# Kernel tuning notes

Measured on AMD Instinct MI355X. Metric: run time of the kernel, lower is better.

The kernel has to match this reference:

```python
import jax, jax.numpy as jnp
import numpy as np

B, L, H, K = 16, 512, 1024, 8192

def setup_inputs() -> dict:
    key = jax.random.key(0)
    k1, k2 = jax.random.split(key)
    inputs = jax.random.normal(k1, (B, L, H), dtype=jnp.float32)
    masks = jnp.ones((B, L), dtype=bool)
    # xavier_uniform for Linear(hidden_size, labels_num): weight [K, H]
    limit = float(np.sqrt(6.0 / (H + K)))
    W = jax.random.uniform(k2, (K, H), dtype=jnp.float32, minval=-limit, maxval=limit)
    return {"inputs": inputs, "masks": masks, "W": W}

def reference(inputs, masks, W):
    # scores: [B, K, L] = (inputs @ W.T).transpose(1,2)
    scores = jnp.einsum('blh,kh->bkl', inputs, W)
    scores = jnp.where(masks[:, None, :], scores, -jnp.inf)
    attn = jax.nn.softmax(scores, axis=-1)          # softmax over L
    return jnp.einsum('bkl,blh->bkh', attn, inputs)  # [B, K, H]
```

## Files before the change

kernel.cpp:

```cpp
#include <hip/hip_runtime.h>
#include <stdint.h>

#define BN 16
#define LN 512
#define HN 1024
#define KN 8192
#define TK 64
#define NTHREADS 512

typedef float  f32x4  __attribute__((ext_vector_type(4)));
typedef __bf16 bf16x8 __attribute__((ext_vector_type(8)));
typedef __bf16 bf16x4 __attribute__((ext_vector_type(4)));

__device__ __forceinline__ void cp16(const void* g, void* l) {
  __builtin_amdgcn_global_load_lds(
      (const __attribute__((address_space(1))) unsigned int*)g,
      (__attribute__((address_space(3))) unsigned int*)l, 16, 0, 0);
}

__global__ void cvt_w(const float* __restrict__ W, __bf16* __restrict__ Wb) {
  const size_t i = (size_t)blockIdx.x * blockDim.x + threadIdx.x;
  const float4 v = ((const float4*)W)[i];
  bf16x4 o; o[0] = (__bf16)v.x; o[1] = (__bf16)v.y; o[2] = (__bf16)v.z; o[3] = (__bf16)v.w;
  ((bf16x4*)Wb)[i] = o;
}

__global__ void trans_x(const float* __restrict__ X, __bf16* __restrict__ Xb,
                        __bf16* __restrict__ Xt) {
  __shared__ __bf16 T[64][72];
  const int b  = blockIdx.y;
  const int l0 = (blockIdx.x & 7) * 64;
  const int h0 = (blockIdx.x >> 3) * 64;
  const int t  = threadIdx.x;
  #pragma unroll
  for (int it = 0; it < 4; ++it) {
    const int idx = it * 256 + t;
    const int lr = idx >> 4, hc = (idx & 15) << 2;
    const float4 v = *(const float4*)(X + ((size_t)b * LN + l0 + lr) * HN + h0 + hc);
    bf16x4 o; o[0] = (__bf16)v.x; o[1] = (__bf16)v.y; o[2] = (__bf16)v.z; o[3] = (__bf16)v.w;
    *(bf16x4*)(Xb + ((size_t)b * LN + l0 + lr) * HN + h0 + hc) = o;
    *(bf16x4*)&T[lr][hc] = o;
  }
  __syncthreads();
  #pragma unroll
  for (int it = 0; it < 4; ++it) {
    const int idx = it * 256 + t;
    const int hr = idx >> 4, lg = (idx & 15) << 2;
    bf16x4 o;
    o[0] = T[lg + 0][hr]; o[1] = T[lg + 1][hr];
    o[2] = T[lg + 2][hr]; o[3] = T[lg + 3][hr];
    *(bf16x4*)(Xt + ((size_t)b * HN + h0 + hr) * LN + l0 + lg) = o;
  }
}

#define P2_AT_LDA 520

struct __align__(16) P1Mem {
  __bf16 xs[2][512 * 64];
  __bf16 wt[2][64 * 64];
};
struct __align__(16) P2Mem {
  __bf16 attn[TK][P2_AT_LDA];
  __bf16 xt[2][512 * 32];
};
struct __align__(16) SMem {
  union {
    P1Mem p1;
    P2Mem p2;
    float osm[TK * 516];
  } u;
  float redM[8][TK];
  float redS[8][TK];
  float Mf[TK];
  float Sinv[TK];
};

__global__ __launch_bounds__(NTHREADS, 1)
void mlattn_fused2(const __bf16* __restrict__ Wb, const __bf16* __restrict__ Xb,
                   const __bf16* __restrict__ Xt, const int* __restrict__ Mk,
                   float* __restrict__ out) {
  __shared__ SMem sm;
  const int t    = threadIdx.x;
  const int wv   = t >> 6;
  const int lane = t & 63;
  const int q    = lane >> 4;
  const int c    = lane & 15;
  const int b    = blockIdx.y;
  const int k0   = blockIdx.x * TK;
  const __bf16* Xbb = Xb + (size_t)b * LN * HN;
  const __bf16* Xtb = Xt + (size_t)b * HN * LN;
  const f32x4 fzero = {0.f, 0.f, 0.f, 0.f};

  const int tr8 = t >> 3, tc8 = t & 7;
  const int colOff1 = ((tc8 ^ (tr8 & 7)) << 3);
  const __bf16* xsrc = Xbb + (size_t)tr8 * HN + colOff1;
  const __bf16* wsrc = Wb + (size_t)(k0 + tr8) * HN + colOff1;
  const int tr4 = t >> 2, tc4 = t & 3;
  const int colOff2 = ((tc4 ^ ((t >> 3) & 3)) << 3);
  const __bf16* tsrc = Xtb + (size_t)tr4 * LN + colOff2;

  f32x4 acc[4][4];
  #pragma unroll
  for (int mt = 0; mt < 4; ++mt)
    #pragma unroll
    for (int nt = 0; nt < 4; ++nt) acc[mt][nt] = fzero;

  const int lw0 = wv * 64;

  {
    cp16(wsrc, &sm.u.p1.wt[0][t * 8]);
    #pragma unroll
    for (int i = 0; i < 8; ++i)
      cp16(xsrc + (size_t)i * 64 * HN, &sm.u.p1.xs[0][(i * 512 + t) * 8]);
  }
  __syncthreads();

  int cur = 0;
  for (int tt = 0; tt < 16; ++tt) {
    if (tt + 1 < 16) {
      const int h0 = (tt + 1) * 64;
      cp16(wsrc + h0, &sm.u.p1.wt[cur ^ 1][t * 8]);
      #pragma unroll
      for (int i = 0; i < 8; ++i)
        cp16(xsrc + (size_t)i * 64 * HN + h0, &sm.u.p1.xs[cur ^ 1][(i * 512 + t) * 8]);
    }
    #pragma unroll
    for (int ks = 0; ks < 2; ++ks) {
      bf16x8 aF[4], bF[4];
      #pragma unroll
      for (int mt = 0; mt < 4; ++mt) {
        const int r = mt * 16 + c;
        aF[mt] = *(const bf16x8*)&sm.u.p1.wt[cur][r * 64 + (((ks * 4 + q) ^ (c & 7)) << 3)];
      }
      #pragma unroll
      for (int nt = 0; nt < 4; ++nt) {
        const int r = lw0 + nt * 16 + c;
        bF[nt] = *(const bf16x8*)&sm.u.p1.xs[cur][r * 64 + (((ks * 4 + q) ^ (c & 7)) << 3)];
      }
      #pragma unroll
      for (int mt = 0; mt < 4; ++mt)
        #pragma unroll
        for (int nt = 0; nt < 4; ++nt)
          acc[mt][nt] = __builtin_amdgcn_mfma_f32_16x16x32_bf16(aF[mt], bF[nt], acc[mt][nt], 0, 0, 0);
    }
    __syncthreads();
    cur ^= 1;
  }

  {
    #pragma unroll
    for (int i = 0; i < 4; ++i)
      cp16(tsrc + (size_t)i * 128 * LN, &sm.u.p2.xt[0][(i * 512 + t) * 8]);
  }

  #pragma unroll
  for (int nt = 0; nt < 4; ++nt) {
    const int m = Mk[b * LN + lw0 + nt * 16 + c];
    if (!m) {
      #pragma unroll
      for (int mt = 0; mt < 4; ++mt)
        #pragma unroll
        for (int r = 0; r < 4; ++r) acc[mt][nt][r] = -1e30f;
    }
  }
  float pm[4][4];
  #pragma unroll
  for (int mt = 0; mt < 4; ++mt)
    #pragma unroll
    for (int r = 0; r < 4; ++r)
      pm[mt][r] = fmaxf(fmaxf(acc[mt][0][r], acc[mt][1][r]), fmaxf(acc[mt][2][r], acc[mt][3][r]));
  #pragma unroll
  for (int off = 1; off < 16; off <<= 1)
    #pragma unroll
    for (int mt = 0; mt < 4; ++mt)
      #pragma unroll
      for (int r = 0; r < 4; ++r)
        pm[mt][r] = fmaxf(pm[mt][r], __shfl_xor(pm[mt][r], off, 64));
  if (c == 0) {
    #pragma unroll
    for (int mt = 0; mt < 4; ++mt)
      #pragma unroll
      for (int r = 0; r < 4; ++r) sm.redM[wv][mt * 16 + q * 4 + r] = pm[mt][r];
  }
  __syncthreads();
  if (t < TK) {
    float m = sm.redM[0][t];
    #pragma unroll
    for (int w = 1; w < 8; ++w) m = fmaxf(m, sm.redM[w][t]);
    sm.Mf[t] = m;
  }
  __syncthreads();

  float ps[4][4];
  #pragma unroll
  for (int mt = 0; mt < 4; ++mt)
    #pragma unroll
    for (int r = 0; r < 4; ++r) {
      const float M = sm.Mf[mt * 16 + q * 4 + r];
      float s = 0.f;
      #pragma unroll
      for (int nt = 0; nt < 4; ++nt) {
        const float e = __expf(acc[mt][nt][r] - M);
        acc[mt][nt][r] = e;
        s += e;
      }
      ps[mt][r] = s;
    }
  #pragma unroll
  for (int off = 1; off < 16; off <<= 1)
    #pragma unroll
    for (int mt = 0; mt < 4; ++mt)
      #pragma unroll
      for (int r = 0; r < 4; ++r) ps[mt][r] += __shfl_xor(ps[mt][r], off, 64);
  if (c == 0) {
    #pragma unroll
    for (int mt = 0; mt < 4; ++mt)
      #pragma unroll
      for (int r = 0; r < 4; ++r) sm.redS[wv][mt * 16 + q * 4 + r] = ps[mt][r];
  }
  __syncthreads();
  if (t < TK) {
    float s = 0.f;
    #pragma unroll
    for (int w = 0; w < 8; ++w) s += sm.redS[w][t];
    sm.Sinv[t] = 1.f / s;
  }
  __syncthreads();

  #pragma unroll
  for (int mt = 0; mt < 4; ++mt)
    #pragma unroll
    for (int r = 0; r < 4; ++r) {
      const int row = mt * 16 + q * 4 + r;
      const float inv = sm.Sinv[row];
      #pragma unroll
      for (int nt = 0; nt < 4; ++nt)
        sm.u.p2.attn[row][lw0 + nt * 16 + c] = (__bf16)(acc[mt][nt][r] * inv);
    }
  __syncthreads();

  const int wM = wv >> 2;
  const int wN = wv & 3;
  const int swq8 = ((q ^ ((c >> 1) & 3)) << 3);
  f32x4 acc2[2][16];
  #pragma unroll
  for (int i = 0; i < 2; ++i)
    #pragma unroll
    for (int j = 0; j < 16; ++j) acc2[i][j] = fzero;

  cur = 0;
  for (int s = 0; s < 32; ++s) {
    if (s + 1 < 32) {
      const int sn = s + 1;
      const __bf16* src = tsrc + (size_t)((sn & 1) * 512) * LN + ((sn >> 1) << 5);
      #pragma unroll
      for (int i = 0; i < 4; ++i)
        cp16(src + (size_t)i * 128 * LN, &sm.u.p2.xt[cur ^ 1][(i * 512 + t) * 8]);
    }
    const int l0c = (s >> 1) << 5;
    const int hh  = s & 1;
    bf16x8 aF2[2], bF2[8];
    #pragma unroll
    for (int mt = 0; mt < 2; ++mt)
      aF2[mt] = *(const bf16x8*)&sm.u.p2.attn[wM * 32 + mt * 16 + c][l0c + q * 8];
    #pragma unroll
    for (int nt = 0; nt < 8; ++nt) {
      const int r = wN * 128 + nt * 16 + c;
      bF2[nt] = *(const bf16x8*)&sm.u.p2.xt[cur][r * 32 + swq8];
    }
    #pragma unroll
    for (int mt = 0; mt < 2; ++mt)
      #pragma unroll
      for (int nt = 0; nt < 8; ++nt)
        acc2[mt][hh * 8 + nt] =
            __builtin_amdgcn_mfma_f32_16x16x32_bf16(aF2[mt], bF2[nt], acc2[mt][hh * 8 + nt], 0, 0, 0);
    __syncthreads();
    cur ^= 1;
  }

  float* outb = out + ((size_t)b * KN + k0) * HN;
  #pragma unroll
  for (int hh = 0; hh < 2; ++hh) {
    if (hh) __syncthreads();
    #pragma unroll
    for (int mt = 0; mt < 2; ++mt)
      #pragma unroll
      for (int nt = 0; nt < 8; ++nt) {
        const int hl = wN * 128 + nt * 16 + c;
        #pragma unroll
        for (int r = 0; r < 4; ++r) {
          const int krow = wM * 32 + mt * 16 + q * 4 + r;
          sm.u.osm[krow * 516 + hl] = acc2[mt][hh * 8 + nt][r];
        }
      }
    __syncthreads();
    #pragma unroll
    for (int i = 0; i < 16; ++i) {
      const int s = i * 512 + t;
      const int row = s >> 7, col4 = s & 127;
      *(f32x4*)(outb + (size_t)row * HN + hh * 512 + (col4 << 2)) =
          *(const f32x4*)&sm.u.osm[row * 516 + (col4 << 2)];
    }
  }
}

#define XT_LDA 72
#define WT_LDA 72
#define AT_LDA_O 520
#define X2_LDA 72

struct __align__(16) SMemOld {
  __bf16 attn[TK][AT_LDA_O];
  union {
    struct { __bf16 xt[LN][XT_LDA]; __bf16 wt[TK][WT_LDA]; } p1;
    __bf16 x2[512][X2_LDA];
  } u;
  float redM[8][TK];
  float redS[8][TK];
  float Mf[TK];
  float Sinv[TK];
};

__device__ __forceinline__ bf16x4 cvt4o(float4 v) {
  bf16x4 r;
  r[0] = (__bf16)v.x; r[1] = (__bf16)v.y; r[2] = (__bf16)v.z; r[3] = (__bf16)v.w;
  return r;
}

__global__ __launch_bounds__(NTHREADS, 2)
void mlattn_fused(const float* __restrict__ X, const int* __restrict__ Mk,
                  const float* __restrict__ W, float* __restrict__ out) {
  __shared__ SMemOld sm;
  const int t    = threadIdx.x;
  const int wv   = t >> 6;
  const int lane = t & 63;
  const int q    = lane >> 4;
  const int c    = lane & 15;
  const int b    = blockIdx.y;
  const int k0   = blockIdx.x * TK;
  const float* Xb = X + (size_t)b * LN * HN;
  const f32x4 fzero = {0.f, 0.f, 0.f, 0.f};

  f32x4 acc[4][4];
  #pragma unroll
  for (int mt = 0; mt < 4; ++mt)
    #pragma unroll
    for (int nt = 0; nt < 4; ++nt) acc[mt][nt] = fzero;

  const int lw0 = wv * 64;
  const int sr  = t >> 4;
  const int sc  = t & 15;

  for (int h0 = 0; h0 < HN; h0 += 64) {
    #pragma unroll
    for (int p = 0; p < 2; ++p) {
      const int row = p * 32 + sr;
      float4 v = *(const float4*)(W + (size_t)(k0 + row) * HN + h0 + sc * 4);
      *(bf16x4*)&sm.u.p1.wt[row][sc * 4] = cvt4o(v);
    }
    #pragma unroll
    for (int p = 0; p < 16; ++p) {
      const int row = p * 32 + sr;
      float4 v = *(const float4*)(Xb + (size_t)row * HN + h0 + sc * 4);
      *(bf16x4*)&sm.u.p1.xt[row][sc * 4] = cvt4o(v);
    }
    __syncthreads();
    #pragma unroll
    for (int ks = 0; ks < 2; ++ks) {
      bf16x8 aF[4], bF[4];
      #pragma unroll
      for (int mt = 0; mt < 4; ++mt)
        aF[mt] = *(const bf16x8*)&sm.u.p1.wt[mt * 16 + c][ks * 32 + q * 8];
      #pragma unroll
      for (int nt = 0; nt < 4; ++nt)
        bF[nt] = *(const bf16x8*)&sm.u.p1.xt[lw0 + nt * 16 + c][ks * 32 + q * 8];
      #pragma unroll
      for (int mt = 0; mt < 4; ++mt)
        #pragma unroll
        for (int nt = 0; nt < 4; ++nt)
          acc[mt][nt] = __builtin_amdgcn_mfma_f32_16x16x32_bf16(aF[mt], bF[nt], acc[mt][nt], 0, 0, 0);
    }
    __syncthreads();
  }

  #pragma unroll
  for (int nt = 0; nt < 4; ++nt) {
    const int m = Mk[b * LN + lw0 + nt * 16 + c];
    if (!m) {
      #pragma unroll
      for (int mt = 0; mt < 4; ++mt)
        #pragma unroll
        for (int r = 0; r < 4; ++r) acc[mt][nt][r] = -1e30f;
    }
  }

  float pm[4][4];
  #pragma unroll
  for (int mt = 0; mt < 4; ++mt)
    #pragma unroll
    for (int r = 0; r < 4; ++r)
      pm[mt][r] = fmaxf(fmaxf(acc[mt][0][r], acc[mt][1][r]), fmaxf(acc[mt][2][r], acc[mt][3][r]));
  #pragma unroll
  for (int off = 1; off < 16; off <<= 1)
    #pragma unroll
    for (int mt = 0; mt < 4; ++mt)
      #pragma unroll
      for (int r = 0; r < 4; ++r)
        pm[mt][r] = fmaxf(pm[mt][r], __shfl_xor(pm[mt][r], off, 64));
  if (c == 0) {
    #pragma unroll
    for (int mt = 0; mt < 4; ++mt)
      #pragma unroll
      for (int r = 0; r < 4; ++r) sm.redM[wv][mt * 16 + q * 4 + r] = pm[mt][r];
  }
  __syncthreads();
  if (t < TK) {
    float m = sm.redM[0][t];
    #pragma unroll
    for (int w = 1; w < 8; ++w) m = fmaxf(m, sm.redM[w][t]);
    sm.Mf[t] = m;
  }
  __syncthreads();

  float ps[4][4];
  #pragma unroll
  for (int mt = 0; mt < 4; ++mt)
    #pragma unroll
    for (int r = 0; r < 4; ++r) {
      const float M = sm.Mf[mt * 16 + q * 4 + r];
      float s = 0.f;
      #pragma unroll
      for (int nt = 0; nt < 4; ++nt) {
        const float e = __expf(acc[mt][nt][r] - M);
        acc[mt][nt][r] = e;
        s += e;
      }
      ps[mt][r] = s;
    }
  #pragma unroll
  for (int off = 1; off < 16; off <<= 1)
    #pragma unroll
    for (int mt = 0; mt < 4; ++mt)
      #pragma unroll
      for (int r = 0; r < 4; ++r) ps[mt][r] += __shfl_xor(ps[mt][r], off, 64);
  if (c == 0) {
    #pragma unroll
    for (int mt = 0; mt < 4; ++mt)
      #pragma unroll
      for (int r = 0; r < 4; ++r) sm.redS[wv][mt * 16 + q * 4 + r] = ps[mt][r];
  }
  __syncthreads();
  if (t < TK) {
    float s = 0.f;
    #pragma unroll
    for (int w = 0; w < 8; ++w) s += sm.redS[w][t];
    sm.Sinv[t] = 1.f / s;
  }
  __syncthreads();

  #pragma unroll
  for (int mt = 0; mt < 4; ++mt)
    #pragma unroll
    for (int r = 0; r < 4; ++r) {
      const int row = mt * 16 + q * 4 + r;
      const float inv = sm.Sinv[row];
      #pragma unroll
      for (int nt = 0; nt < 4; ++nt)
        sm.attn[row][lw0 + nt * 16 + c] = (__bf16)(acc[mt][nt][r] * inv);
    }

  const int wM = wv >> 2;
  const int wN = wv & 3;
  f32x4 acc2[2][16];
  #pragma unroll
  for (int i = 0; i < 2; ++i)
    #pragma unroll
    for (int j = 0; j < 16; ++j) acc2[i][j] = fzero;

  for (int lc = 0; lc < 8; ++lc) {
    const int l0c = lc * 64;
    #pragma unroll
    for (int hh = 0; hh < 2; ++hh) {
      __syncthreads();
      {
        const float* xcol = Xb + (size_t)hh * 512 + t;
        #pragma unroll
        for (int u = 0; u < 16; ++u) {
          const int l = l0c + u * 4;
          const float d0 = xcol[(size_t)(l + 0) * HN];
          const float d1 = xcol[(size_t)(l + 1) * HN];
          const float d2 = xcol[(size_t)(l + 2) * HN];
          const float d3 = xcol[(size_t)(l + 3) * HN];
          bf16x4 p;
          p[0] = (__bf16)d0; p[1] = (__bf16)d1; p[2] = (__bf16)d2; p[3] = (__bf16)d3;
          *(bf16x4*)&sm.u.x2[t][u * 4] = p;
        }
      }
      __syncthreads();
      #pragma unroll
      for (int ks = 0; ks < 2; ++ks) {
        bf16x8 aF2[2], bF2[8];
        #pragma unroll
        for (int mt = 0; mt < 2; ++mt)
          aF2[mt] = *(const bf16x8*)&sm.attn[wM * 32 + mt * 16 + c][l0c + ks * 32 + q * 8];
        #pragma unroll
        for (int nt = 0; nt < 8; ++nt)
          bF2[nt] = *(const bf16x8*)&sm.u.x2[wN * 128 + nt * 16 + c][ks * 32 + q * 8];
        #pragma unroll
        for (int mt = 0; mt < 2; ++mt)
          #pragma unroll
          for (int nt = 0; nt < 8; ++nt)
            acc2[mt][hh * 8 + nt] =
                __builtin_amdgcn_mfma_f32_16x16x32_bf16(aF2[mt], bF2[nt], acc2[mt][hh * 8 + nt], 0, 0, 0);
      }
    }
  }

  float* outb = out + ((size_t)b * KN + k0) * HN;
  #pragma unroll
  for (int mt = 0; mt < 2; ++mt) {
    #pragma unroll
    for (int j = 0; j < 16; ++j) {
      const int hh = j >> 3, nt = j & 7;
      const int h = hh * 512 + wN * 128 + nt * 16 + c;
      #pragma unroll
      for (int r = 0; r < 4; ++r) {
        const int krow = wM * 32 + mt * 16 + q * 4 + r;
        outb[(size_t)krow * HN + h] = acc2[mt][j][r];
      }
    }
  }
}

extern "C" void kernel_launch(void* const* d_in, const int* in_sizes, int n_in,
                              void* d_out, int out_size, void* d_ws, size_t ws_size,
                              hipStream_t stream) {
  (void)in_sizes; (void)n_in; (void)out_size;
  const float* X = (const float*)d_in[0];
  const int* Mk = (const int*)d_in[1];
  const float* W = (const float*)d_in[2];
  float* out = (float*)d_out;

  const size_t need = ((size_t)KN * HN + 2 * (size_t)BN * LN * HN) * sizeof(__bf16);
  if (d_ws == nullptr || ws_size < need) {
    dim3 grid(KN / TK, BN);
    mlattn_fused<<<grid, NTHREADS, 0, stream>>>(X, Mk, W, out);
    return;
  }

  __bf16* Wb = (__bf16*)d_ws;
  __bf16* Xbb = Wb + (size_t)KN * HN;
  __bf16* Xtb = Xbb + (size_t)BN * LN * HN;

  cvt_w<<<(KN * HN / 4) / 256, 256, 0, stream>>>(W, Wb);
  trans_x<<<dim3(128, BN), 256, 0, stream>>>(X, Xbb, Xtb);
  mlattn_fused2<<<dim3(KN / TK, BN), NTHREADS, 0, stream>>>(Wb, Xbb, Xtb, Mk, out);
}
```

Measured before the change: 1.001 ms.

## Pipeline GEMM stages with partial vmcnt waits, raw barriers and MFMA priority

Restructures both matmul loops in the fused kernel so the next tile's global-to-LDS copies are issued before waiting. Each loop waits only on the older loads using explicit s_waitcnt vmcnt counts and raw s_barrier instead of __syncthreads, and raises wave priority around the MFMA blocks. The mask load is hoisted to the kernel start. The aim is to hide load latency and avoid full-drain waits at every barrier. This relies on hand-counted vmcnt values and scheduling fences, which are fragile if the number of outstanding loads per thread changes.

```diff
diff --git a/kernel.cpp b/kernel.cpp
--- a/kernel.cpp
+++ b/kernel.cpp
@@ -17,6 +17,9 @@
       (const __attribute__((address_space(1))) unsigned int*)g,
       (__attribute__((address_space(3))) unsigned int*)l, 16, 0, 0);
 }
+
+#define SFENCE() __builtin_amdgcn_sched_barrier(0)
+#define WAVE_BARRIER() __builtin_amdgcn_s_barrier()
 
 __global__ void cvt_w(const float* __restrict__ W, __bf16* __restrict__ Wb) {
   const size_t i = (size_t)blockIdx.x * blockDim.x + threadIdx.x;
@@ -75,6 +78,53 @@
   float Sinv[TK];
 };
 
+__device__ __forceinline__ void p1_mfma(const __bf16* __restrict__ wtb,
+                                        const __bf16* __restrict__ xsb,
+                                        int c, int q, int lw0,
+                                        f32x4 (&acc)[4][4]) {
+  #pragma unroll
+  for (int ks = 0; ks < 2; ++ks) {
+    bf16x8 aF[4], bF[4];
+    #pragma unroll
+    for (int mt = 0; mt < 4; ++mt) {
+      const int r = mt * 16 + c;
+      aF[mt] = *(const bf16x8*)&wtb[r * 64 + (((ks * 4 + q) ^ (c & 7)) << 3)];
+    }
+    #pragma unroll
+    for (int nt = 0; nt < 4; ++nt) {
+      const int r = lw0 + nt * 16 + c;
+      bF[nt] = *(const bf16x8*)&xsb[r * 64 + (((ks * 4 + q) ^ (c & 7)) << 3)];
+    }
+    #pragma unroll
+    for (int mt = 0; mt < 4; ++mt)
+      #pragma unroll
+      for (int nt = 0; nt < 4; ++nt)
+        acc[mt][nt] = __builtin_amdgcn_mfma_f32_16x16x32_bf16(aF[mt], bF[nt], acc[mt][nt], 0, 0, 0);
+  }
+}
+
+template <int HH>
+__device__ __forceinline__ void p2_mfma(const __bf16 (*attn)[P2_AT_LDA],
+                                        const __bf16* __restrict__ xtb,
+                                        int c, int q, int wM, int wN, int l0c,
+                                        int swq8, f32x4 (&acc2)[2][16]) {
+  bf16x8 aF2[2], bF2[8];
+  #pragma unroll
+  for (int mt = 0; mt < 2; ++mt)
+    aF2[mt] = *(const bf16x8*)&attn[wM * 32 + mt * 16 + c][l0c + q * 8];
+  #pragma unroll
+  for (int nt = 0; nt < 8; ++nt) {
+    const int r = wN * 128 + nt * 16 + c;
+    bF2[nt] = *(const bf16x8*)&xtb[r * 32 + swq8];
+  }
+  #pragma unroll
+  for (int mt = 0; mt < 2; ++mt)
+    #pragma unroll
+    for (int nt = 0; nt < 8; ++nt)
+      acc2[mt][HH * 8 + nt] =
+          __builtin_amdgcn_mfma_f32_16x16x32_bf16(aF2[mt], bF2[nt], acc2[mt][HH * 8 + nt], 0, 0, 0);
+}
+
 __global__ __launch_bounds__(NTHREADS, 1)
 void mlattn_fused2(const __bf16* __restrict__ Wb, const __bf16* __restrict__ Xb,
                    const __bf16* __restrict__ Xt, const int* __restrict__ Mk,
@@ -90,6 +140,12 @@
   const __bf16* Xbb = Xb + (size_t)b * LN * HN;
   const __bf16* Xtb = Xt + (size_t)b * HN * LN;
   const f32x4 fzero = {0.f, 0.f, 0.f, 0.f};
+  const int lw0 = wv * 64;
+
+  int mkv[4];
+  #pragma unroll
+  for (int nt = 0; nt < 4; ++nt) mkv[nt] = Mk[b * LN + lw0 + nt * 16 + c];
+  asm volatile("" : "+v"(mkv[0]), "+v"(mkv[1]), "+v"(mkv[2]), "+v"(mkv[3]));
 
   const int tr8 = t >> 3, tc8 = t & 7;
   const int colOff1 = ((tc8 ^ (tr8 & 7)) << 3);
@@ -105,58 +161,47 @@
     #pragma unroll
     for (int nt = 0; nt < 4; ++nt) acc[mt][nt] = fzero;
 
-  const int lw0 = wv * 64;
-
-  {
-    cp16(wsrc, &sm.u.p1.wt[0][t * 8]);
+  cp16(wsrc, &sm.u.p1.wt[1][t * 8]);
+  #pragma unroll
+  for (int i = 0; i < 8; ++i)
+    cp16(xsrc + (size_t)i * 64 * HN, &sm.u.p1.xs[1][(i * 512 + t) * 8]);
+  SFENCE();
+
+  #pragma unroll 1
+  for (int tt = 0; tt < 15; ++tt) {
+    const int bc = (tt + 1) & 1;
+    const int h0 = (tt + 1) * 64;
+    cp16(wsrc + h0, &sm.u.p1.wt[bc ^ 1][t * 8]);
     #pragma unroll
     for (int i = 0; i < 8; ++i)
-      cp16(xsrc + (size_t)i * 64 * HN, &sm.u.p1.xs[0][(i * 512 + t) * 8]);
-  }
-  __syncthreads();
-
-  int cur = 0;
-  for (int tt = 0; tt < 16; ++tt) {
-    if (tt + 1 < 16) {
-      const int h0 = (tt + 1) * 64;
-      cp16(wsrc + h0, &sm.u.p1.wt[cur ^ 1][t * 8]);
-      #pragma unroll
-      for (int i = 0; i < 8; ++i)
-        cp16(xsrc + (size_t)i * 64 * HN + h0, &sm.u.p1.xs[cur ^ 1][(i * 512 + t) * 8]);
-    }
-    #pragma unroll
-    for (int ks = 0; ks < 2; ++ks) {
-      bf16x8 aF[4], bF[4];
-      #pragma unroll
-      for (int mt = 0; mt < 4; ++mt) {
-        const int r = mt * 16 + c;
-        aF[mt] = *(const bf16x8*)&sm.u.p1.wt[cur][r * 64 + (((ks * 4 + q) ^ (c & 7)) << 3)];
-      }
-      #pragma unroll
-      for (int nt = 0; nt < 4; ++nt) {
-        const int r = lw0 + nt * 16 + c;
-        bF[nt] = *(const bf16x8*)&sm.u.p1.xs[cur][r * 64 + (((ks * 4 + q) ^ (c & 7)) << 3)];
-      }
-      #pragma unroll
-      for (int mt = 0; mt < 4; ++mt)
-        #pragma unroll
-        for (int nt = 0; nt < 4; ++nt)
-          acc[mt][nt] = __builtin_amdgcn_mfma_f32_16x16x32_bf16(aF[mt], bF[nt], acc[mt][nt], 0, 0, 0);
-    }
-    __syncthreads();
-    cur ^= 1;
-  }
-
-  {
-    #pragma unroll
-    for (int i = 0; i < 4; ++i)
-      cp16(tsrc + (size_t)i * 128 * LN, &sm.u.p2.xt[0][(i * 512 + t) * 8]);
-  }
+      cp16(xsrc + (size_t)i * 64 * HN + h0, &sm.u.p1.xs[bc ^ 1][(i * 512 + t) * 8]);
+    SFENCE();
+    asm volatile("s_waitcnt vmcnt(9)" ::: "memory");
+    SFENCE();
+    WAVE_BARRIER();
+    SFENCE();
+    __builtin_amdgcn_s_setprio(1);
+    p1_mfma(sm.u.p1.wt[bc], sm.u.p1.xs[bc], c, q, lw0, acc);
+    __builtin_amdgcn_s_setprio(0);
+    SFENCE();
+    WAVE_BARRIER();
+    SFENCE();
+  }
+  #pragma unroll
+  for (int i = 0; i < 4; ++i)
+    cp16(tsrc + (size_t)i * 128 * LN, &sm.u.p2.xt[0][(i * 512 + t) * 8]);
+  SFENCE();
+  asm volatile("s_waitcnt vmcnt(4)" ::: "memory");
+  SFENCE();
+  WAVE_BARRIER();
+  SFENCE();
+  __builtin_amdgcn_s_setprio(1);
+  p1_mfma(sm.u.p1.wt[0], sm.u.p1.xs[0], c, q, lw0, acc);
+  __builtin_amdgcn_s_setprio(0);
 
   #pragma unroll
   for (int nt = 0; nt < 4; ++nt) {
-    const int m = Mk[b * LN + lw0 + nt * 16 + c];
-    if (!m) {
+    if (!mkv[nt]) {
       #pragma unroll
       for (int mt = 0; mt < 4; ++mt)
         #pragma unroll
@@ -248,35 +293,44 @@
     #pragma unroll
     for (int j = 0; j < 16; ++j) acc2[i][j] = fzero;
 
-  cur = 0;
-  for (int s = 0; s < 32; ++s) {
-    if (s + 1 < 32) {
-      const int sn = s + 1;
-      const __bf16* src = tsrc + (size_t)((sn & 1) * 512) * LN + ((sn >> 1) << 5);
-      #pragma unroll
-      for (int i = 0; i < 4; ++i)
-        cp16(src + (size_t)i * 128 * LN, &sm.u.p2.xt[cur ^ 1][(i * 512 + t) * 8]);
-    }
-    const int l0c = (s >> 1) << 5;
-    const int hh  = s & 1;
-    bf16x8 aF2[2], bF2[8];
-    #pragma unroll
-    for (int mt = 0; mt < 2; ++mt)
-      aF2[mt] = *(const bf16x8*)&sm.u.p2.attn[wM * 32 + mt * 16 + c][l0c + q * 8];
-    #pragma unroll
-    for (int nt = 0; nt < 8; ++nt) {
-      const int r = wN * 128 + nt * 16 + c;
-      bF2[nt] = *(const bf16x8*)&sm.u.p2.xt[cur][r * 32 + swq8];
-    }
-    #pragma unroll
-    for (int mt = 0; mt < 2; ++mt)
-      #pragma unroll
-      for (int nt = 0; nt < 8; ++nt)
-        acc2[mt][hh * 8 + nt] =
-            __builtin_amdgcn_mfma_f32_16x16x32_bf16(aF2[mt], bF2[nt], acc2[mt][hh * 8 + nt], 0, 0, 0);
-    __syncthreads();
-    cur ^= 1;
-  }
+#define P2STEP(BUF, S)                                                          \
+  {                                                                             \
+    const int sn_ = (S) + 1;                                                    \
+    const __bf16* src_ =                                                        \
+        tsrc + (size_t)((sn_ & 1) * 512) * LN + ((sn_ >> 1) << 5);              \
+    _Pragma("unroll")                                                           \
+    for (int i_ = 0; i_ < 4; ++i_)                                              \
+      cp16(src_ + (size_t)i_ * 128 * LN,                                        \
+           &sm.u.p2.xt[(BUF) ^ 1][(i_ * 512 + t) * 8]);                         \
+    SFENCE();                                                                   \
+    asm volatile("s_waitcnt vmcnt(4)" ::: "memory");                            \
+    SFENCE();                                                                   \
+    WAVE_BARRIER();                                                             \
+    SFENCE();                                                                   \
+    __builtin_amdgcn_s_setprio(1);                                              \
+    p2_mfma<(BUF)>(sm.u.p2.attn, sm.u.p2.xt[(BUF)], c, q, wM, wN,               \
+                   ((S) >> 1) << 5, swq8, acc2);                                \
+    __builtin_amdgcn_s_setprio(0);                                              \
+    SFENCE();                                                                   \
+    WAVE_BARRIER();                                                             \
+    SFENCE();                                                                   \
+  }
+
+  #pragma unroll 1
+  for (int s = 0; s < 30; s += 2) {
+    P2STEP(0, s);
+    P2STEP(1, s + 1);
+  }
+  P2STEP(0, 30);
+  asm volatile("s_waitcnt vmcnt(0)" ::: "memory");
+  SFENCE();
+  WAVE_BARRIER();
+  SFENCE();
+  __builtin_amdgcn_s_setprio(1);
+  p2_mfma<1>(sm.u.p2.attn, sm.u.p2.xt[1], c, q, wM, wN, 480, swq8, acc2);
+  __builtin_amdgcn_s_setprio(0);
+  __syncthreads();
+#undef P2STEP
 
   float* outb = out + ((size_t)b * KN + k0) * HN;
   #pragma unroll
```

Measured after the change: 964.6 us. -3.7%, faster.
